# Optimization experiments

Measured on AMD Instinct MI355X. Metric: run time of the kernel, lower is better.

The kernel has to match this reference:

```python
import jax, jax.numpy as jnp
import numpy as np

L_IN, L_ENC, B = 1024, 1024, 16
D_IN, D_ENC, D_EMB = 512, 512, 512


def setup_inputs() -> dict:
    key = jax.random.key(0)
    ks = jax.random.split(key, 9)
    s_in = 1.0 / np.sqrt(D_IN)
    s_emb = 1.0 / np.sqrt(D_EMB)
    s_enc = 1.0 / np.sqrt(D_ENC)
    return {
        "in_seq": jax.random.normal(ks[0], (L_IN, B, D_IN), jnp.float32),
        "enc_seq": jax.random.normal(ks[1], (L_ENC, B, D_ENC), jnp.float32),
        "prev_target_seq": jax.random.normal(ks[2], (L_IN, B, D_EMB), jnp.float32),
        # torch Linear weights: (out_features, in_features)
        "W_in2enc": jax.random.normal(ks[3], (D_ENC, D_IN), jnp.float32) * s_in,
        "b_in2enc": jnp.zeros((D_ENC,), jnp.float32),
        "W_lab2enc": jax.random.normal(ks[4], (D_ENC, D_EMB), jnp.float32) * s_emb,
        "b_lab2enc": jnp.zeros((D_ENC,), jnp.float32),
        "W_enc2in": jax.random.normal(ks[5], (D_IN, D_ENC), jnp.float32) * s_enc,
        "b_enc2in": jnp.zeros((D_IN,), jnp.float32),
    }


def reference(in_seq, enc_seq, prev_target_seq,
              W_in2enc, b_in2enc, W_lab2enc, b_lab2enc, W_enc2in, b_enc2in):
    # d_vals: (L_in, B, D_enc) = proj(in_seq) + proj(prev_target_seq)
    in_proj = jnp.einsum('lbi,ei->lbe', in_seq, W_in2enc) + b_in2enc
    tgt_proj = jnp.einsum('lbm,em->lbe', prev_target_seq, W_lab2enc) + b_lab2enc
    d_vals = in_proj + tgt_proj
    # raw attention scores: (L_in, L_enc, B) dot products over D_enc
    scores = jnp.einsum('lbe,mbe->lmb', d_vals, enc_seq)
    # sum-normalization (NOT softmax) over the encoder-length axis
    attn = scores / jnp.sum(scores, axis=1, keepdims=True)
    # weighted sum of encoder states: (L_in, B, D_enc)
    context = jnp.einsum('lmb,mbe->lbe', attn, enc_seq)
    # project back to input dim
    return jnp.einsum('lbe,ie->lbi', context, W_enc2in) + b_enc2in
```

## Files before the change

kernel.cpp:

```cpp
#include <hip/hip_runtime.h>
#include <cstdint>

static constexpr int LDR = 8192;

typedef uint16_t u16;
typedef __attribute__((ext_vector_type(8))) short short8;
typedef __attribute__((ext_vector_type(4))) float f32x4;
struct alignas(8) U16x4 { u16 x, y, z, w; };

__device__ __forceinline__ u16 f2bf(float f) {
    union { float f; unsigned u; } v; v.f = f;
    unsigned r = v.u + 0x7fffu + ((v.u >> 16) & 1u);
    return (u16)(r >> 16);
}

__device__ __forceinline__ short8 cvt8(const float4 a, const float4 b) {
    short8 r;
    r[0]=(short)f2bf(a.x); r[1]=(short)f2bf(a.y); r[2]=(short)f2bf(a.z); r[3]=(short)f2bf(a.w);
    r[4]=(short)f2bf(b.x); r[5]=(short)f2bf(b.y); r[6]=(short)f2bf(b.z); r[7]=(short)f2bf(b.w);
    return r;
}

template<int MODE>
__device__ __forceinline__ const short8* a_ptr(const u16* A, int row, int kk, int z) {
    if constexpr (MODE == 1)      return (const short8*)(A + row*1024 + kk);
    else if constexpr (MODE == 5) return (const short8*)(A + z*524288 + row*1024 + kk);
    else if constexpr (MODE == 6) return (const short8*)(A + row*512 + kk);
    else                          return (const short8*)(A + (row*16 + z)*512 + kk);
}
template<int MODE>
__device__ __forceinline__ const short8* b_ptr(const u16* B, int row, int kk, int z) {
    if constexpr (MODE == 1)      return (const short8*)(B + row*1024 + kk);
    else if constexpr (MODE == 5) return (const short8*)(B + z*524288 + row*1024 + kk);
    else if constexpr (MODE == 6) return (const short8*)(B + z*262144 + row*512 + kk);
    else                          return (const short8*)(B + z*262144 + row*512 + kk);
}

template<int MODE>
__global__ __launch_bounds__(256) void gemm_bf16(
    const u16* __restrict__ A, const u16* __restrict__ Bm,
    const float* __restrict__ b1, const float* __restrict__ b2,
    const float* __restrict__ b3, const float* __restrict__ Sinv,
    u16* __restrict__ Cb, float* __restrict__ Cf)
{
    constexpr int K = (MODE == 1 || MODE == 5) ? 1024 : 512;
    __shared__ __align__(16) u16 As[128 * 40];
    __shared__ __align__(16) u16 Bs[128 * 40];
    const int z    = blockIdx.z;
    const int row0 = blockIdx.y * 128;
    const int col0 = blockIdx.x * 128;
    const int tid  = threadIdx.x;
    const int lane = tid & 63, w = tid >> 6;
    const int wm = w >> 1, wn = w & 1;
    const int quad = lane >> 4, l16 = lane & 15;
    const int crow = tid >> 2, ck8 = (tid & 3) * 8;

    f32x4 acc[4][4] = {};
    short8 pa0 = *a_ptr<MODE>(A,  row0+crow,    ck8, z);
    short8 pa1 = *a_ptr<MODE>(A,  row0+crow+64, ck8, z);
    short8 pb0 = *b_ptr<MODE>(Bm, col0+crow,    ck8, z);
    short8 pb1 = *b_ptr<MODE>(Bm, col0+crow+64, ck8, z);

    for (int kb = 0; kb < K; kb += 32) {
        *(short8*)&As[crow*40 + ck8]      = pa0;
        *(short8*)&As[(crow+64)*40 + ck8] = pa1;
        *(short8*)&Bs[crow*40 + ck8]      = pb0;
        *(short8*)&Bs[(crow+64)*40 + ck8] = pb1;
        __syncthreads();
        if (kb + 32 < K) {
            const int kn = kb + 32 + ck8;
            pa0 = *a_ptr<MODE>(A,  row0+crow,    kn, z);
            pa1 = *a_ptr<MODE>(A,  row0+crow+64, kn, z);
            pb0 = *b_ptr<MODE>(Bm, col0+crow,    kn, z);
            pb1 = *b_ptr<MODE>(Bm, col0+crow+64, kn, z);
        }
        short8 af[4], bfr[4];
        #pragma unroll
        for (int i = 0; i < 4; ++i)
            af[i] = *(const short8*)&As[(wm*64 + i*16 + l16)*40 + quad*8];
        #pragma unroll
        for (int j = 0; j < 4; ++j)
            bfr[j] = *(const short8*)&Bs[(wn*64 + j*16 + l16)*40 + quad*8];
        #pragma unroll
        for (int i = 0; i < 4; ++i)
            #pragma unroll
            for (int j = 0; j < 4; ++j)
                acc[i][j] = __builtin_amdgcn_mfma_f32_16x16x32_bf16(af[i], bfr[j], acc[i][j], 0, 0, 0);
        __syncthreads();
    }

    #pragma unroll
    for (int i = 0; i < 4; ++i) {
        const int grow = row0 + wm*64 + i*16 + quad*4;
        #pragma unroll
        for (int j = 0; j < 4; ++j) {
            const int gcol = col0 + wn*64 + j*16 + l16;
            #pragma unroll
            for (int r = 0; r < 4; ++r) {
                float v = acc[i][j][r];
                const int R = grow + r;
                if constexpr (MODE == 1) {
                    v += b1[gcol] + b2[gcol];
                    Cb[R*512 + gcol] = f2bf(v);
                } else if constexpr (MODE == 5 || MODE == 6) {
                    Cb[z*262144 + R*512 + gcol] = f2bf(v);
                } else {
                    const float s = Sinv[R*16 + z];
                    Cf[(R*16 + z)*512 + gcol] = v * s + b3[gcol];
                }
            }
        }
    }
}

__global__ __launch_bounds__(256) void enct_kernel(
    const float* __restrict__ E, u16* __restrict__ EncT, double* __restrict__ part)
{
    __shared__ float tile[64][65];
    __shared__ double sred[256];
    const int bb = blockIdx.z;
    const int m0 = blockIdx.y * 64;
    const int e0 = blockIdx.x * 64;
    const int t = threadIdx.x;
    const int tr = t >> 4;
    const int tc4 = (t & 15) * 4;
    #pragma unroll
    for (int it = 0; it < 4; ++it) {
        const int ml = tr + it*16;
        float4 v = *(const float4*)&E[(m0+ml)*LDR + bb*512 + e0 + tc4];
        *(float4*)&tile[ml][tc4] = v;
    }
    __syncthreads();
    #pragma unroll
    for (int it = 0; it < 4; ++it) {
        const int el = tr + it*16;
        U16x4 o;
        o.x = f2bf(tile[tc4+0][el]);
        o.y = f2bf(tile[tc4+1][el]);
        o.z = f2bf(tile[tc4+2][el]);
        o.w = f2bf(tile[tc4+3][el]);
        *(U16x4*)&EncT[bb*524288 + (e0+el)*1024 + m0 + tc4] = o;
    }
    const int el = t & 63, mq = t >> 6;
    double a = 0.0;
    #pragma unroll
    for (int j = 0; j < 16; ++j) a += (double)tile[mq*16 + j][el];
    sred[t] = a;
    __syncthreads();
    if (t < 64) {
        double s = sred[t] + sred[t+64] + sred[t+128] + sred[t+192];
        part[blockIdx.y*8192 + bb*512 + e0 + t] = s;
    }
}

__global__ __launch_bounds__(256) void prep_small(
    const float* __restrict__ W1, const float* __restrict__ W2,
    const float* __restrict__ W3, const float* __restrict__ b1,
    const float* __restrict__ b2, const double* __restrict__ part,
    u16* __restrict__ W12, u16* __restrict__ W3b,
    double* __restrict__ u, double* __restrict__ cd)
{
    const int blk = blockIdx.x, tid = threadIdx.x;
    if (blk < 384) {
        const int idx = blk*256 + tid;
        if (idx < 65536) {
            const int r = idx >> 7, k8 = (idx & 127) * 8;
            const float* src = (k8 < 512) ? (W1 + r*512 + k8) : (W2 + r*512 + (k8 - 512));
            float4 a = *(const float4*)src;
            float4 b = *((const float4*)src + 1);
            *(short8*)&W12[r*1024 + k8] = cvt8(a, b);
        } else {
            const int i2 = idx - 65536;
            const int r = i2 >> 6, k8 = (i2 & 63) * 8;
            const float* src = W3 + r*512 + k8;
            float4 a = *(const float4*)src;
            float4 b = *((const float4*)src + 1);
            *(short8*)&W3b[r*512 + k8] = cvt8(a, b);
        }
        return;
    }
    __shared__ double es_l[512];
    __shared__ double red[256];
    int b;
    if (blk < 448) b = ((blk - 384) & 31) >> 1;
    else           b = blk - 448;
    for (int e = tid; e < 512; e += 256) {
        double s = 0.0;
        #pragma unroll
        for (int c = 0; c < 16; ++c) s += part[c*8192 + b*512 + e];
        es_l[e] = s;
    }
    __syncthreads();
    if (blk < 448) {
        const int blk2 = blk - 384;
        const int which = blk2 >> 5;
        const int t = (blk2 & 31)*256 + tid;
        const int i = t & 511;
        const float* W = which ? W2 : W1;
        double a = 0.0;
        for (int e = 0; e < 512; ++e) a += (double)W[e*512 + i] * es_l[e];
        u[which*8192 + t] = a;
    } else {
        double a = 0.0;
        for (int e = tid; e < 512; e += 256) a += (double)(b1[e] + b2[e]) * es_l[e];
        red[tid] = a; __syncthreads();
        for (int s = 128; s > 0; s >>= 1) { if (tid < s) red[tid] += red[tid+s]; __syncthreads(); }
        if (tid == 0) cd[b] = red[0];
    }
}

__global__ __launch_bounds__(256) void s_xt_kernel(
    const float* __restrict__ X, const float* __restrict__ T,
    const double* __restrict__ u, const double* __restrict__ cd,
    float* __restrict__ Sinv, u16* __restrict__ XT)
{
    const int wave = threadIdx.x >> 6, lane = threadIdx.x & 63;
    const int r = blockIdx.x * 4 + wave;
    const int b = r & 15;
    const double* u1 = u + b*512;
    const double* u2 = u + 8192 + b*512;
    const int e = lane * 8;
    float4 x0 = *(const float4*)&X[r*512 + e];
    float4 x1 = *(const float4*)&X[r*512 + e + 4];
    float4 t0 = *(const float4*)&T[r*512 + e];
    float4 t1 = *(const float4*)&T[r*512 + e + 4];
    double a = 0.0;
    a += (double)x0.x*u1[e+0] + (double)x0.y*u1[e+1] + (double)x0.z*u1[e+2] + (double)x0.w*u1[e+3];
    a += (double)x1.x*u1[e+4] + (double)x1.y*u1[e+5] + (double)x1.z*u1[e+6] + (double)x1.w*u1[e+7];
    a += (double)t0.x*u2[e+0] + (double)t0.y*u2[e+1] + (double)t0.z*u2[e+2] + (double)t0.w*u2[e+3];
    a += (double)t1.x*u2[e+4] + (double)t1.y*u2[e+5] + (double)t1.z*u2[e+6] + (double)t1.w*u2[e+7];
    *(short8*)&XT[r*1024 + e]       = cvt8(x0, x1);
    *(short8*)&XT[r*1024 + 512 + e] = cvt8(t0, t1);
    #pragma unroll
    for (int off = 32; off > 0; off >>= 1) a += __shfl_down(a, off, 64);
    if (lane == 0) Sinv[r] = (float)(1.0 / (a + cd[b]));
}

extern "C" void kernel_launch(void* const* d_in, const int* in_sizes, int n_in,
                              void* d_out, int out_size, void* d_ws, size_t ws_size,
                              hipStream_t stream)
{
    const float* X   = (const float*)d_in[0];
    const float* Enc = (const float*)d_in[1];
    const float* T   = (const float*)d_in[2];
    const float* W1  = (const float*)d_in[3];
    const float* b1  = (const float*)d_in[4];
    const float* W2  = (const float*)d_in[5];
    const float* b2  = (const float*)d_in[6];
    const float* W3  = (const float*)d_in[7];
    const float* b3  = (const float*)d_in[8];
    float* out = (float*)d_out;

    char* w = (char*)d_ws;
    u16*    dvals_bf = (u16*)(w);
    u16*    EncT_bf  = (u16*)(w + 16777216);
    u16*    Gram_bf  = (u16*)(w + 33554432);
    u16*    HT_bf    = (u16*)(w + 41943040);
    u16*    W12      = (u16*)(w + 50331648);
    u16*    W3b      = (u16*)(w + 51380224);
    double* part     = (double*)(w + 51904512);
    double* u        = (double*)(w + 52953088);
    double* cd       = (double*)(w + 53084160);
    float*  Sinv     = (float*)(w + 53084288);
    u16*    XTb      = (u16*)d_out;

    dim3 blk(256);
    enct_kernel <<<dim3(8, 16, 16), blk, 0, stream>>>(Enc, EncT_bf, part);
    prep_small  <<<dim3(464),       blk, 0, stream>>>(W1, W2, W3, b1, b2, part, W12, W3b, u, cd);
    s_xt_kernel <<<dim3(4096),      blk, 0, stream>>>(X, T, u, cd, Sinv, XTb);

    gemm_bf16<5><<<dim3(4, 4, 16),  blk, 0, stream>>>(EncT_bf, EncT_bf, b1, b2, b3, Sinv, Gram_bf, out);
    gemm_bf16<6><<<dim3(4, 4, 16),  blk, 0, stream>>>(W3b, Gram_bf, b1, b2, b3, Sinv, HT_bf, out);
    gemm_bf16<1><<<dim3(4, 128, 1), blk, 0, stream>>>(XTb, W12, b1, b2, b3, Sinv, dvals_bf, out);
    gemm_bf16<4><<<dim3(4, 8, 16),  blk, 0, stream>>>(dvals_bf, HT_bf, b1, b2, b3, Sinv, dvals_bf, out);
}
```

Baseline: 271.5 us.

## Use async global-to-LDS loads with double buffering and swizzled LDS in GEMMs

Replaces the register-staged GEMM mainloop with direct global_load_lds_dwordx4 transfers into double-buffered, XOR-swizzled LDS tiles, using a K step of 64. Modes 5 and 6 get 64-row tiles so their grids have twice as many blocks. The s_xt kernel now caches the per-batch u vectors in registers and processes 8 rows per wave, launching fewer blocks. The goal is to overlap global loads with MFMA work and cut register/LDS store traffic, at the cost of more LDS use and lower occupancy.

```diff
diff --git a/kernel.cpp b/kernel.cpp
--- a/kernel.cpp
+++ b/kernel.cpp
@@ -21,80 +21,112 @@
     return r;
 }
 
+__device__ __forceinline__ void gl_lds16(const u16* g, unsigned ldsaddr) {
+    asm volatile("s_mov_b32 m0, %0\n\t"
+                 "global_load_lds_dwordx4 %1, off"
+                 :: "s"(__builtin_amdgcn_readfirstlane(ldsaddr)), "v"(g)
+                 : "memory");
+}
+
 template<int MODE>
-__device__ __forceinline__ const short8* a_ptr(const u16* A, int row, int kk, int z) {
-    if constexpr (MODE == 1)      return (const short8*)(A + row*1024 + kk);
-    else if constexpr (MODE == 5) return (const short8*)(A + z*524288 + row*1024 + kk);
-    else if constexpr (MODE == 6) return (const short8*)(A + row*512 + kk);
-    else                          return (const short8*)(A + (row*16 + z)*512 + kk);
-}
-template<int MODE>
-__device__ __forceinline__ const short8* b_ptr(const u16* B, int row, int kk, int z) {
-    if constexpr (MODE == 1)      return (const short8*)(B + row*1024 + kk);
-    else if constexpr (MODE == 5) return (const short8*)(B + z*524288 + row*1024 + kk);
-    else if constexpr (MODE == 6) return (const short8*)(B + z*262144 + row*512 + kk);
-    else                          return (const short8*)(B + z*262144 + row*512 + kk);
-}
-
-template<int MODE>
-__global__ __launch_bounds__(256) void gemm_bf16(
+__global__ __launch_bounds__(256) void gemm_async(
     const u16* __restrict__ A, const u16* __restrict__ Bm,
     const float* __restrict__ b1, const float* __restrict__ b2,
     const float* __restrict__ b3, const float* __restrict__ Sinv,
     u16* __restrict__ Cb, float* __restrict__ Cf)
 {
-    constexpr int K = (MODE == 1 || MODE == 5) ? 1024 : 512;
-    __shared__ __align__(16) u16 As[128 * 40];
-    __shared__ __align__(16) u16 Bs[128 * 40];
+    constexpr int K   = (MODE == 1 || MODE == 5) ? 1024 : 512;
+    constexpr int BM  = (MODE == 5 || MODE == 6) ? 64 : 128;
+    constexpr int NJ  = (BM == 128) ? 4 : 2;
+    constexpr int NIA = BM / 32;
+    constexpr int NIB = 4;
+    constexpr int ASZ = BM * 128;
+    constexpr int BSZ = 128 * 128;
+    constexpr int LDA = (MODE == 1) ? 1024 : (MODE == 4) ? 8192 : (MODE == 5) ? 1024 : 512;
+    constexpr int LDB = (MODE == 1 || MODE == 5) ? 1024 : 512;
+
+    __shared__ __align__(16) u16 lds[(2*ASZ + 2*BSZ) / 2];
+
     const int z    = blockIdx.z;
-    const int row0 = blockIdx.y * 128;
+    const int row0 = blockIdx.y * BM;
     const int col0 = blockIdx.x * 128;
     const int tid  = threadIdx.x;
-    const int lane = tid & 63, w = tid >> 6;
-    const int wm = w >> 1, wn = w & 1;
-    const int quad = lane >> 4, l16 = lane & 15;
-    const int crow = tid >> 2, ck8 = (tid & 3) * 8;
-
-    f32x4 acc[4][4] = {};
-    short8 pa0 = *a_ptr<MODE>(A,  row0+crow,    ck8, z);
-    short8 pa1 = *a_ptr<MODE>(A,  row0+crow+64, ck8, z);
-    short8 pb0 = *b_ptr<MODE>(Bm, col0+crow,    ck8, z);
-    short8 pb1 = *b_ptr<MODE>(Bm, col0+crow+64, ck8, z);
-
-    for (int kb = 0; kb < K; kb += 32) {
-        *(short8*)&As[crow*40 + ck8]      = pa0;
-        *(short8*)&As[(crow+64)*40 + ck8] = pa1;
-        *(short8*)&Bs[crow*40 + ck8]      = pb0;
-        *(short8*)&Bs[(crow+64)*40 + ck8] = pb1;
+    const int l    = tid & 63, w = tid >> 6;
+    const int wm   = (BM == 128) ? (w >> 1) : 0;
+    const int wn   = (BM == 128) ? (w & 1) : w;
+    const int quad = l >> 4, l16 = l & 15;
+
+    const u16* Ab = A;
+    const u16* Bb = Bm;
+    if constexpr (MODE == 4) Ab = A + z*512;
+    if constexpr (MODE == 5) { Ab = A + z*524288; Bb = Bm + z*524288; }
+    if constexpr (MODE == 6) Bb = Bm + z*262144;
+    if constexpr (MODE == 4) Bb = Bm + z*262144;
+
+    const int lq = l >> 3;
+    const int loffu = ((l & 7) ^ lq) * 8;
+    const u16* gA[NIA];
+    #pragma unroll
+    for (int i = 0; i < NIA; ++i)
+        gA[i] = Ab + (size_t)(row0 + i*32 + w*8 + lq) * LDA + loffu;
+    const u16* gB[NIB];
+    #pragma unroll
+    for (int i = 0; i < NIB; ++i)
+        gB[i] = Bb + (size_t)(col0 + i*32 + w*8 + lq) * LDB + loffu;
+
+    const unsigned lbase = (unsigned)(size_t)&lds[0];
+
+    auto stage = [&](int c) {
+        #pragma unroll
+        for (int i = 0; i < NIA; ++i) {
+            gl_lds16(gA[i], lbase + c*ASZ + i*4096 + w*1024);
+            gA[i] += 64;
+        }
+        #pragma unroll
+        for (int i = 0; i < NIB; ++i) {
+            gl_lds16(gB[i], lbase + 2*ASZ + c*BSZ + i*4096 + w*1024);
+            gB[i] += 64;
+        }
+    };
+
+    f32x4 acc[4][NJ] = {};
+    const int swzr = (l16 & 7) << 3;
+    const int arow = wm * 64;
+    const int brow = wn * (BM == 128 ? 64 : 32);
+
+    stage(0);
+    int cur = 0;
+    for (int kb = 0; kb < K; kb += 64) {
+        asm volatile("s_waitcnt vmcnt(0)" ::: "memory");
         __syncthreads();
-        if (kb + 32 < K) {
-            const int kn = kb + 32 + ck8;
-            pa0 = *a_ptr<MODE>(A,  row0+crow,    kn, z);
-            pa1 = *a_ptr<MODE>(A,  row0+crow+64, kn, z);
-            pb0 = *b_ptr<MODE>(Bm, col0+crow,    kn, z);
-            pb1 = *b_ptr<MODE>(Bm, col0+crow+64, kn, z);
-        }
-        short8 af[4], bfr[4];
-        #pragma unroll
-        for (int i = 0; i < 4; ++i)
-            af[i] = *(const short8*)&As[(wm*64 + i*16 + l16)*40 + quad*8];
-        #pragma unroll
-        for (int j = 0; j < 4; ++j)
-            bfr[j] = *(const short8*)&Bs[(wn*64 + j*16 + l16)*40 + quad*8];
-        #pragma unroll
-        for (int i = 0; i < 4; ++i)
+        if (kb + 64 < K) stage(cur ^ 1);
+        const int abase = cur * (ASZ/2);
+        const int bbase = ASZ + cur * (BSZ/2);
+        #pragma unroll
+        for (int kk = 0; kk < 2; ++kk) {
+            const int koff = (kk*32 + quad*8) ^ swzr;
+            short8 af[4], bfr[NJ];
             #pragma unroll
-            for (int j = 0; j < 4; ++j)
-                acc[i][j] = __builtin_amdgcn_mfma_f32_16x16x32_bf16(af[i], bfr[j], acc[i][j], 0, 0, 0);
-        __syncthreads();
+            for (int i = 0; i < 4; ++i)
+                af[i] = *(const short8*)&lds[abase + (arow + i*16 + l16)*64 + koff];
+            #pragma unroll
+            for (int j = 0; j < NJ; ++j)
+                bfr[j] = *(const short8*)&lds[bbase + (brow + j*16 + l16)*64 + koff];
+            #pragma unroll
+            for (int i = 0; i < 4; ++i)
+                #pragma unroll
+                for (int j = 0; j < NJ; ++j)
+                    acc[i][j] = __builtin_amdgcn_mfma_f32_16x16x32_bf16(af[i], bfr[j], acc[i][j], 0, 0, 0);
+        }
+        cur ^= 1;
     }
 
     #pragma unroll
     for (int i = 0; i < 4; ++i) {
-        const int grow = row0 + wm*64 + i*16 + quad*4;
-        #pragma unroll
-        for (int j = 0; j < 4; ++j) {
-            const int gcol = col0 + wn*64 + j*16 + l16;
+        const int grow = row0 + arow + i*16 + quad*4;
+        #pragma unroll
+        for (int j = 0; j < NJ; ++j) {
+            const int gcol = col0 + brow + j*16 + l16;
             #pragma unroll
             for (int r = 0; r < 4; ++r) {
                 float v = acc[i][j][r];
@@ -215,25 +247,34 @@
     float* __restrict__ Sinv, u16* __restrict__ XT)
 {
     const int wave = threadIdx.x >> 6, lane = threadIdx.x & 63;
-    const int r = blockIdx.x * 4 + wave;
-    const int b = r & 15;
-    const double* u1 = u + b*512;
-    const double* u2 = u + 8192 + b*512;
+    const int b = blockIdx.x & 15, g = blockIdx.x >> 4;
     const int e = lane * 8;
-    float4 x0 = *(const float4*)&X[r*512 + e];
-    float4 x1 = *(const float4*)&X[r*512 + e + 4];
-    float4 t0 = *(const float4*)&T[r*512 + e];
-    float4 t1 = *(const float4*)&T[r*512 + e + 4];
-    double a = 0.0;
-    a += (double)x0.x*u1[e+0] + (double)x0.y*u1[e+1] + (double)x0.z*u1[e+2] + (double)x0.w*u1[e+3];
-    a += (double)x1.x*u1[e+4] + (double)x1.y*u1[e+5] + (double)x1.z*u1[e+6] + (double)x1.w*u1[e+7];
-    a += (double)t0.x*u2[e+0] + (double)t0.y*u2[e+1] + (double)t0.z*u2[e+2] + (double)t0.w*u2[e+3];
-    a += (double)t1.x*u2[e+4] + (double)t1.y*u2[e+5] + (double)t1.z*u2[e+6] + (double)t1.w*u2[e+7];
-    *(short8*)&XT[r*1024 + e]       = cvt8(x0, x1);
-    *(short8*)&XT[r*1024 + 512 + e] = cvt8(t0, t1);
-    #pragma unroll
-    for (int off = 32; off > 0; off >>= 1) a += __shfl_down(a, off, 64);
-    if (lane == 0) Sinv[r] = (float)(1.0 / (a + cd[b]));
+    double u1r[8], u2r[8];
+    #pragma unroll
+    for (int k = 0; k < 8; ++k) {
+        u1r[k] = u[b*512 + e + k];
+        u2r[k] = u[8192 + b*512 + e + k];
+    }
+    const double cb = cd[b];
+    #pragma unroll 2
+    for (int i = 0; i < 8; ++i) {
+        const int j = g*32 + wave*8 + i;
+        const int r = j*16 + b;
+        float4 x0 = *(const float4*)&X[r*512 + e];
+        float4 x1 = *(const float4*)&X[r*512 + e + 4];
+        float4 t0 = *(const float4*)&T[r*512 + e];
+        float4 t1 = *(const float4*)&T[r*512 + e + 4];
+        double a = 0.0;
+        a += (double)x0.x*u1r[0] + (double)x0.y*u1r[1] + (double)x0.z*u1r[2] + (double)x0.w*u1r[3];
+        a += (double)x1.x*u1r[4] + (double)x1.y*u1r[5] + (double)x1.z*u1r[6] + (double)x1.w*u1r[7];
+        a += (double)t0.x*u2r[0] + (double)t0.y*u2r[1] + (double)t0.z*u2r[2] + (double)t0.w*u2r[3];
+        a += (double)t1.x*u2r[4] + (double)t1.y*u2r[5] + (double)t1.z*u2r[6] + (double)t1.w*u2r[7];
+        *(short8*)&XT[r*1024 + e]       = cvt8(x0, x1);
+        *(short8*)&XT[r*1024 + 512 + e] = cvt8(t0, t1);
+        #pragma unroll
+        for (int off = 32; off > 0; off >>= 1) a += __shfl_down(a, off, 64);
+        if (lane == 0) Sinv[r] = (float)(1.0 / (a + cb));
+    }
 }
 
 extern "C" void kernel_launch(void* const* d_in, const int* in_sizes, int n_in,
@@ -267,10 +308,10 @@
     dim3 blk(256);
     enct_kernel <<<dim3(8, 16, 16), blk, 0, stream>>>(Enc, EncT_bf, part);
     prep_small  <<<dim3(464),       blk, 0, stream>>>(W1, W2, W3, b1, b2, part, W12, W3b, u, cd);
-    s_xt_kernel <<<dim3(4096),      blk, 0, stream>>>(X, T, u, cd, Sinv, XTb);
-
-    gemm_bf16<5><<<dim3(4, 4, 16),  blk, 0, stream>>>(EncT_bf, EncT_bf, b1, b2, b3, Sinv, Gram_bf, out);
-    gemm_bf16<6><<<dim3(4, 4, 16),  blk, 0, stream>>>(W3b, Gram_bf, b1, b2, b3, Sinv, HT_bf, out);
-    gemm_bf16<1><<<dim3(4, 128, 1), blk, 0, stream>>>(XTb, W12, b1, b2, b3, Sinv, dvals_bf, out);
-    gemm_bf16<4><<<dim3(4, 8, 16),  blk, 0, stream>>>(dvals_bf, HT_bf, b1, b2, b3, Sinv, dvals_bf, out);
-}
+    s_xt_kernel <<<dim3(512),       blk, 0, stream>>>(X, T, u, cd, Sinv, XTb);
+
+    gemm_async<5><<<dim3(4, 8, 16),  blk, 0, stream>>>(EncT_bf, EncT_bf, b1, b2, b3, Sinv, Gram_bf, out);
+    gemm_async<6><<<dim3(4, 8, 16),  blk, 0, stream>>>(W3b, Gram_bf, b1, b2, b3, Sinv, HT_bf, out);
+    gemm_async<1><<<dim3(4, 128, 1), blk, 0, stream>>>(XTb, W12, b1, b2, b3, Sinv, dvals_bf, out);
+    gemm_async<4><<<dim3(4, 8, 16),  blk, 0, stream>>>(dvals_bf, HT_bf, b1, b2, b3, Sinv, dvals_bf, out);
+}
```

New measurement: 247.6 us. 8.8% less time.
